# Performance work log

Measured on AMD Instinct MI355X. Metric: run time of the kernel, lower is better.

The kernel has to match this reference:

```python
import jax, jax.numpy as jnp
import numpy as np
from jax import lax

N_NODES = 100000
N_EDGES = 600000  # even: edges stored as consecutive reverse pairs
NODE_F = 64
EDGE_F = 16
EDGE_H = 128
NODE_H = 128
NUM_STEPS = 6


def setup_inputs() -> dict:
    key = jax.random.key(0)
    ks = jax.random.split(key, 16)
    # paired reverse edges: edge 2k is (src,dst), edge 2k+1 is (dst,src)
    src = jax.random.randint(ks[0], (N_EDGES // 2,), 0, N_NODES, dtype=jnp.int32)
    dst = jax.random.randint(ks[1], (N_EDGES // 2,), 0, N_NODES, dtype=jnp.int32)
    from_nodes = jnp.stack([src, dst], axis=1).reshape(-1)
    to_nodes = jnp.stack([dst, src], axis=1).reshape(-1)
    edges = jnp.stack([from_nodes, to_nodes], axis=0)
    return {
        "node_features": jax.random.normal(ks[2], (N_NODES, NODE_F), jnp.float32),
        "edge_features": jax.random.normal(ks[3], (N_EDGES, EDGE_F), jnp.float32),
        "edge_hiddens": jnp.zeros((N_EDGES, EDGE_H), jnp.float32),
        "edges": edges,
        "W1_w": jax.random.normal(ks[4], (NODE_F, EDGE_H), jnp.float32) / np.sqrt(NODE_F),
        "W1_b": jnp.zeros((EDGE_H,), jnp.float32),
        "W2_w": jax.random.normal(ks[5], (EDGE_F, EDGE_H), jnp.float32) / np.sqrt(EDGE_F),
        "W2_b": jnp.zeros((EDGE_H,), jnp.float32),
        "W3_w": jax.random.normal(ks[6], (EDGE_H, EDGE_H), jnp.float32) / np.sqrt(EDGE_H),
        "W3_b": jnp.zeros((EDGE_H,), jnp.float32),
        "U1_w": jax.random.normal(ks[7], (NODE_F, NODE_H), jnp.float32) / np.sqrt(NODE_F),
        "U1_b": jnp.zeros((NODE_H,), jnp.float32),
        "U2_w": jax.random.normal(ks[8], (EDGE_H, NODE_H), jnp.float32) / np.sqrt(EDGE_H),
        "U2_b": jnp.zeros((NODE_H,), jnp.float32),
    }


def reference(node_features, edge_features, edge_hiddens, edges,
              W1_w, W1_b, W2_w, W2_b, W3_w, W3_b, U1_w, U1_b, U2_w, U2_b):
    from_nodes = edges[0]
    to_nodes = edges[1]
    n_edges = edges.shape[1]
    # backlink of edge i is its reverse pair: even i -> i+1, odd i -> i-1
    idx = jnp.arange(n_edges)
    backlink = idx + ((idx + 1) % 2) * 2 - 1

    # loop-invariant terms
    W1_x_u = (node_features @ W1_w + W1_b)[from_nodes]     # [E, EH]
    W2_x_uv = edge_features @ W2_w + W2_b                  # [E, EH]

    def step(h, _):
        # sum edge hiddens by source node, gather back per-edge, drop backlink
        s = jax.ops.segment_sum(h, from_nodes, num_segments=N_NODES)  # [N, EH]
        wu = s[from_nodes] - h[backlink]                               # [E, EH]
        h_new = jax.nn.relu(W1_x_u + W2_x_uv + (wu @ W3_w + W3_b))
        return h_new, None

    edge_h, _ = lax.scan(step, edge_hiddens, None, length=NUM_STEPS)

    U1_x_u = node_features @ U1_w + U1_b                   # [N, NH]
    U2_vu = edge_h @ U2_w + U2_b                           # [E, NH]
    agg = jax.ops.segment_sum(U2_vu, to_nodes, num_segments=N_NODES)
    node_hiddens = jax.nn.relu(U1_x_u + agg)               # [N, NH]
    return node_hiddens
```

## Files before the change

kernel.cpp:

```cpp
#include <hip/hip_runtime.h>
#include <hip/hip_bf16.h>

#define N_NODES 100000
#define N_EDGES 600000
#define SCAN_BLOCKS ((N_NODES + 255) / 256)

typedef __bf16 bf16;
typedef __bf16 bf16x2 __attribute__((ext_vector_type(2)));
typedef __bf16 bf16x4 __attribute__((ext_vector_type(4)));
typedef __bf16 bf16x8 __attribute__((ext_vector_type(8)));
typedef float f32x4 __attribute__((ext_vector_type(4)));

__global__ void deg_hist(const int* __restrict__ from, int* __restrict__ deg, int E) {
    int e = blockIdx.x * blockDim.x + threadIdx.x;
    if (e < E) atomicAdd(&deg[from[e]], 1);
}

__global__ __launch_bounds__(256) void block_sums(
    const int* __restrict__ deg, int* __restrict__ bsum)
{
    __shared__ int s[256];
    int i = blockIdx.x * 256 + threadIdx.x;
    s[threadIdx.x] = (i < N_NODES) ? deg[i] : 0;
    __syncthreads();
    for (int st = 128; st > 0; st >>= 1) {
        if (threadIdx.x < st) s[threadIdx.x] += s[threadIdx.x + st];
        __syncthreads();
    }
    if (threadIdx.x == 0) bsum[blockIdx.x] = s[0];
}

__global__ __launch_bounds__(256) void scan_partials(
    const int* __restrict__ bsum, int* __restrict__ bpref, int* __restrict__ off)
{
    __shared__ int s[SCAN_BLOCKS];
    for (int i = threadIdx.x; i < SCAN_BLOCKS; i += 256) s[i] = bsum[i];
    __syncthreads();
    if (threadIdx.x == 0) {
        int run = 0;
        for (int i = 0; i < SCAN_BLOCKS; i++) { int t = s[i]; s[i] = run; run += t; }
        off[N_NODES] = run;
    }
    __syncthreads();
    for (int i = threadIdx.x; i < SCAN_BLOCKS; i += 256) bpref[i] = s[i];
}

__global__ __launch_bounds__(256) void block_scan(
    const int* __restrict__ deg, const int* __restrict__ bpref,
    int* __restrict__ off, int* __restrict__ cursor)
{
    __shared__ int s[256];
    int i = blockIdx.x * 256 + threadIdx.x;
    int v = (i < N_NODES) ? deg[i] : 0;
    s[threadIdx.x] = v;
    __syncthreads();
    for (int st = 1; st < 256; st <<= 1) {
        int x = (threadIdx.x >= st) ? s[threadIdx.x - st] : 0;
        __syncthreads();
        s[threadIdx.x] += x;
        __syncthreads();
    }
    if (i < N_NODES) {
        int o = bpref[blockIdx.x] + s[threadIdx.x] - v;
        off[i] = o;
        cursor[i] = o;
    }
}

__global__ void scatter_csr(const int* __restrict__ from, int* __restrict__ cursor,
                            int* __restrict__ se, int* __restrict__ rank, int E) {
    int e = blockIdx.x * blockDim.x + threadIdx.x;
    if (e < E) {
        int p = atomicAdd(&cursor[from[e]], 1);
        se[p] = e;
        rank[e] = p;
    }
}

__global__ void make_maps(const int* __restrict__ se, const int* __restrict__ from,
                          const int* __restrict__ rank,
                          int* __restrict__ fromP, int* __restrict__ backP, int E) {
    int i = blockIdx.x * blockDim.x + threadIdx.x;
    if (i < E) {
        int e = se[i];
        fromP[i] = from[e];
        backP[i] = rank[e ^ 1];
    }
}

__global__ __launch_bounds__(256) void node_gemm(
    const float* __restrict__ A, const float* __restrict__ B,
    const float* __restrict__ bias, float* __restrict__ C, int M)
{
    __shared__ float As[16][65];
    __shared__ float Bs[16][128];
    int row0 = blockIdx.x * 64;
    int tid = threadIdx.x;
    int tx = tid & 15, ty = tid >> 4;
    float acc[4][8];
    #pragma unroll
    for (int i = 0; i < 4; i++)
        #pragma unroll
        for (int j = 0; j < 8; j++) acc[i][j] = 0.f;

    for (int kk = 0; kk < 64; kk += 16) {
        int m  = tid >> 2;
        int k4 = (tid & 3) * 4;
        float4 v = make_float4(0.f, 0.f, 0.f, 0.f);
        if (row0 + m < M)
            v = *(const float4*)(A + (size_t)(row0 + m) * 64 + kk + k4);
        As[k4 + 0][m] = v.x; As[k4 + 1][m] = v.y;
        As[k4 + 2][m] = v.z; As[k4 + 3][m] = v.w;
        #pragma unroll
        for (int t = 0; t < 2; t++) {
            int id = tid + t * 256;
            int k = id >> 5, n4 = (id & 31) * 4;
            *(float4*)(&Bs[k][n4]) = *(const float4*)(B + (size_t)(kk + k) * 128 + n4);
        }
        __syncthreads();
        #pragma unroll
        for (int k = 0; k < 16; k++) {
            float a[4], b[8];
            #pragma unroll
            for (int i = 0; i < 4; i++) a[i] = As[k][ty * 4 + i];
            #pragma unroll
            for (int j = 0; j < 8; j++) b[j] = Bs[k][tx + j * 16];
            #pragma unroll
            for (int i = 0; i < 4; i++)
                #pragma unroll
                for (int j = 0; j < 8; j++) acc[i][j] += a[i] * b[j];
        }
        __syncthreads();
    }
    #pragma unroll
    for (int i = 0; i < 4; i++) {
        int r = row0 + ty * 4 + i;
        if (r < M) {
            #pragma unroll
            for (int j = 0; j < 8; j++) {
                int c = tx + j * 16;
                C[(size_t)r * 128 + c] = acc[i][j] + bias[c];
            }
        }
    }
}

__global__ __launch_bounds__(256) void base_sorted(
    const float* __restrict__ nodeW1, const int* __restrict__ fromP,
    const int* __restrict__ se, const float* __restrict__ ef,
    const float* __restrict__ W2, const float* __restrict__ W2b,
    const float* __restrict__ W3b, bf16* __restrict__ baseP)
{
    int tid = threadIdx.x;
    int c0 = (tid & 31) * 4;
    int sub = tid >> 5;
    float4 w[16];
    #pragma unroll
    for (int k = 0; k < 16; k++) w[k] = *(const float4*)(W2 + k * 128 + c0);
    float4 bias;
    {
        float4 a = *(const float4*)(W2b + c0);
        float4 b = *(const float4*)(W3b + c0);
        bias = make_float4(a.x + b.x, a.y + b.y, a.z + b.z, a.w + b.w);
    }
    #pragma unroll 1
    for (int it = 0; it < 64; ++it) {
        int i = blockIdx.x * 512 + it * 8 + sub;
        if (i >= N_EDGES) break;
        const float* efr = ef + (size_t)se[i] * 16;
        float4 nv = *(const float4*)(nodeW1 + (size_t)fromP[i] * 128 + c0);
        float4 acc = make_float4(bias.x + nv.x, bias.y + nv.y,
                                 bias.z + nv.z, bias.w + nv.w);
        #pragma unroll
        for (int k = 0; k < 16; k++) {
            float s = efr[k];
            acc.x += s * w[k].x; acc.y += s * w[k].y;
            acc.z += s * w[k].z; acc.w += s * w[k].w;
        }
        bf16x4 o;
        o[0] = (bf16)acc.x; o[1] = (bf16)acc.y; o[2] = (bf16)acc.z; o[3] = (bf16)acc.w;
        *(bf16x4*)(baseP + (size_t)i * 128 + c0) = o;
    }
}

__global__ __launch_bounds__(256) void prep_weights(
    const float* __restrict__ W3, const float* __restrict__ U2,
    bf16* __restrict__ W3T, bf16* __restrict__ U2T)
{
    int i = blockIdx.x * 256 + threadIdx.x;
    if (i < 128 * 128) {
        int k = i >> 7, n = i & 127;
        W3T[n * 128 + k] = (bf16)W3[k * 128 + n];
        U2T[n * 128 + k] = (bf16)U2[k * 128 + n];
    }
}

__global__ __launch_bounds__(256) void edge_mfma_v2(
    const bf16* __restrict__ baseP, const bf16* __restrict__ gin,
    const bf16* __restrict__ S, const int* __restrict__ fromP,
    const int* __restrict__ backP, const bf16* __restrict__ BT,
    bf16* __restrict__ gout, int fused)
{
    __shared__ bf16 Bsw[128 * 128];
    int tid = threadIdx.x;

    #pragma unroll
    for (int t = 0; t < 8; t++) {
        int c = tid + t * 256;
        int cmr = c & 15;
        int cq  = (c >> 4) & 3;
        int ckt = (c >> 6) & 3;
        int cn  = c >> 8;
        int brow = cn * 16 + cmr;
        int bcol = ckt * 32 + cq * 8;
        *(bf16x8*)&Bsw[(size_t)c * 8] =
            *(const bf16x8*)(BT + (size_t)brow * 128 + bcol);
    }
    __syncthreads();

    int wave = tid >> 6, lane = tid & 63;
    int quad = lane >> 4, mr = lane & 15;

    #pragma unroll 1
    for (int it = 0; it < 4; ++it) {
        int i0 = blockIdx.x * 256 + wave * 64 + it * 16;
        if (i0 >= N_EDGES) break;
        int i = i0 + mr;

        bf16x8 afr[4];
        if (!fused) {
            #pragma unroll
            for (int kt = 0; kt < 4; kt++) {
                bf16x8 bb = *(const bf16x8*)(baseP + (size_t)i * 128 + kt * 32 + quad * 8);
                #pragma unroll
                for (int j = 0; j < 8; j++)
                    afr[kt][j] = (bf16)fmaxf((float)bb[j], 0.f);
            }
        } else {
            const bf16* sr = S   + (size_t)fromP[i] * 128;
            const bf16* gr = gin + (size_t)backP[i] * 128;
            #pragma unroll
            for (int kt = 0; kt < 4; kt++) {
                int c = kt * 32 + quad * 8;
                bf16x8 bb = *(const bf16x8*)(baseP + (size_t)i * 128 + c);
                bf16x8 gg = *(const bf16x8*)(gr + c);
                bf16x8 ss = *(const bf16x8*)(sr + c);
                #pragma unroll
                for (int j = 0; j < 8; j++) {
                    float v = (float)bb[j] + (float)ss[j] - (float)gg[j];
                    afr[kt][j] = (bf16)fmaxf(v, 0.f);
                }
            }
        }

        f32x4 acc[8];
        #pragma unroll
        for (int n = 0; n < 8; n++) acc[n] = (f32x4){0.f, 0.f, 0.f, 0.f};
        #pragma unroll
        for (int kt = 0; kt < 4; kt++) {
            #pragma unroll
            for (int n = 0; n < 8; n++) {
                bf16x8 b = *(const bf16x8*)&Bsw[(size_t)(((n * 4 + kt) * 64) + lane) * 8];
                acc[n] = __builtin_amdgcn_mfma_f32_16x16x32_bf16(afr[kt], b, acc[n], 0, 0, 0);
            }
        }

        #pragma unroll
        for (int np = 0; np < 4; np++) {
            int n0 = np * 2;
            #pragma unroll
            for (int reg = 0; reg < 4; reg++) {
                float v0 = acc[n0][reg], v1 = acc[n0 + 1][reg];
                float o0 = __shfl_xor(v0, 1);
                float o1 = __shfl_xor(v1, 1);
                bf16x2 pk;
                int colb;
                if ((mr & 1) == 0) {
                    pk[0] = (bf16)v0; pk[1] = (bf16)o0;
                    colb = n0 * 16 + mr;
                } else {
                    pk[0] = (bf16)o1; pk[1] = (bf16)v1;
                    colb = (n0 + 1) * 16 + (mr ^ 1);
                }
                int row = i0 + quad * 4 + reg;
                *(bf16x2*)(gout + (size_t)row * 128 + colb) = pk;
            }
        }
    }
}

__global__ __launch_bounds__(256) void segsum_stream(
    const bf16* __restrict__ g, const int* __restrict__ off, bf16* __restrict__ S)
{
    int n = blockIdx.x * 4 + (threadIdx.x >> 6);
    if (n >= N_NODES) return;
    int lane = threadIdx.x & 63;
    int o0 = off[n], o1 = off[n + 1];
    float a0 = 0.f, a1 = 0.f;
    for (int i = o0; i < o1; ++i) {
        bf16x2 v = *(const bf16x2*)(g + (size_t)i * 128 + lane * 2);
        a0 += (float)v[0];
        a1 += (float)v[1];
    }
    bf16x2 o; o[0] = (bf16)a0; o[1] = (bf16)a1;
    *(bf16x2*)(S + (size_t)n * 128 + lane * 2) = o;
}

__global__ __launch_bounds__(256) void segsum_final(
    const bf16* __restrict__ g, const int* __restrict__ off,
    const int* __restrict__ backP, float* __restrict__ agg)
{
    int n = blockIdx.x * 4 + (threadIdx.x >> 6);
    if (n >= N_NODES) return;
    int lane = threadIdx.x & 63;
    int o0 = off[n], o1 = off[n + 1];
    float a0 = 0.f, a1 = 0.f;
    for (int i = o0; i < o1; ++i) {
        int e = backP[i];
        bf16x2 v = *(const bf16x2*)(g + (size_t)e * 128 + lane * 2);
        a0 += (float)v[0];
        a1 += (float)v[1];
    }
    *(float2*)(agg + (size_t)n * 128 + lane * 2) = make_float2(a0, a1);
}

__global__ __launch_bounds__(256) void final_out(
    const float* __restrict__ U1x, const float* __restrict__ agg,
    const int* __restrict__ deg, const float* __restrict__ U2b,
    float* __restrict__ out)
{
    int gid = blockIdx.x * 256 + threadIdx.x;
    int n  = gid >> 5;
    if (n >= N_NODES) return;
    int c4 = gid & 31;
    float d = (float)deg[n];
    float4 a  = *(const float4*)(U1x + (size_t)n * 128 + c4 * 4);
    float4 ag = *(const float4*)(agg + (size_t)n * 128 + c4 * 4);
    float4 ub = *(const float4*)(U2b + c4 * 4);
    float4 r;
    r.x = fmaxf(a.x + ag.x + d * ub.x, 0.f);
    r.y = fmaxf(a.y + ag.y + d * ub.y, 0.f);
    r.z = fmaxf(a.z + ag.z + d * ub.z, 0.f);
    r.w = fmaxf(a.w + ag.w + d * ub.w, 0.f);
    *(float4*)(out + (size_t)n * 128 + c4 * 4) = r;
}

extern "C" void kernel_launch(void* const* d_in, const int* in_sizes, int n_in,
                              void* d_out, int out_size, void* d_ws, size_t ws_size,
                              hipStream_t stream) {
    const float* nf  = (const float*)d_in[0];
    const float* ef  = (const float*)d_in[1];
    const int* edges = (const int*)d_in[3];
    const int* from  = edges;
    const float* W1w = (const float*)d_in[4];
    const float* W1b = (const float*)d_in[5];
    const float* W2w = (const float*)d_in[6];
    const float* W2b = (const float*)d_in[7];
    const float* W3w = (const float*)d_in[8];
    const float* W3b = (const float*)d_in[9];
    const float* U1w = (const float*)d_in[10];
    const float* U1b = (const float*)d_in[11];
    const float* U2w = (const float*)d_in[12];
    const float* U2b = (const float*)d_in[13];
    float* out = (float*)d_out;

    const size_t NODE_MAT = (size_t)N_NODES * 128;
    const size_t EDGE_MAT = (size_t)N_EDGES * 128;
    char* w = (char*)d_ws;
    float* nodeW1 = (float*)w; w += NODE_MAT * 4;
    float* agg    = (float*)w; w += NODE_MAT * 4;
    bf16*  S      = (bf16*)w;  w += NODE_MAT * 2;
    bf16*  baseP  = (bf16*)w;  w += EDGE_MAT * 2;
    bf16*  g0     = (bf16*)w;  w += EDGE_MAT * 2;
    bf16*  g1     = (bf16*)w;  w += EDGE_MAT * 2;
    bf16*  W3T    = (bf16*)w;  w += 128 * 128 * 2;
    bf16*  U2T    = (bf16*)w;  w += 128 * 128 * 2;
    int*   deg    = (int*)w;   w += (size_t)N_NODES * 4;
    int*   off    = (int*)w;   w += (size_t)(N_NODES + 1) * 4;
    int*   cursor = (int*)w;   w += (size_t)N_NODES * 4;
    int*   bsum   = (int*)w;   w += (size_t)SCAN_BLOCKS * 4;
    int*   bpref  = (int*)w;   w += (size_t)SCAN_BLOCKS * 4;
    int*   se     = (int*)w;   w += (size_t)N_EDGES * 4;
    int*   rank   = (int*)w;   w += (size_t)N_EDGES * 4;
    int*   fromP  = (int*)w;   w += (size_t)N_EDGES * 4;
    int*   backP  = (int*)w;   w += (size_t)N_EDGES * 4;

    hipMemsetAsync(deg, 0, (size_t)N_NODES * 4, stream);
    deg_hist<<<(N_EDGES + 255) / 256, 256, 0, stream>>>(from, deg, N_EDGES);
    block_sums<<<SCAN_BLOCKS, 256, 0, stream>>>(deg, bsum);
    scan_partials<<<1, 256, 0, stream>>>(bsum, bpref, off);
    block_scan<<<SCAN_BLOCKS, 256, 0, stream>>>(deg, bpref, off, cursor);
    scatter_csr<<<(N_EDGES + 255) / 256, 256, 0, stream>>>(from, cursor, se, rank, N_EDGES);
    make_maps<<<(N_EDGES + 255) / 256, 256, 0, stream>>>(se, from, rank, fromP, backP, N_EDGES);

    prep_weights<<<(128 * 128 + 255) / 256, 256, 0, stream>>>(W3w, U2w, W3T, U2T);
    node_gemm<<<(N_NODES + 63) / 64, 256, 0, stream>>>(nf, W1w, W1b, nodeW1, N_NODES);
    base_sorted<<<(N_EDGES + 511) / 512, 256, 0, stream>>>(
        nodeW1, fromP, se, ef, W2w, W2b, W3b, baseP);

    const int EGRID = (N_EDGES + 255) / 256;
    bf16* G[2] = {g0, g1};
    edge_mfma_v2<<<EGRID, 256, 0, stream>>>(
        baseP, G[0], S, fromP, backP, W3T, G[0], 0);
    segsum_stream<<<(N_NODES + 3) / 4, 256, 0, stream>>>(G[0], off, S);
    int cur = 0;
    for (int it = 1; it < 5; ++it) {
        edge_mfma_v2<<<EGRID, 256, 0, stream>>>(
            baseP, G[cur], S, fromP, backP, W3T, G[cur ^ 1], 1);
        cur ^= 1;
        segsum_stream<<<(N_NODES + 3) / 4, 256, 0, stream>>>(G[cur], off, S);
    }
    edge_mfma_v2<<<EGRID, 256, 0, stream>>>(
        baseP, G[cur], S, fromP, backP, U2T, G[cur ^ 1], 1);
    cur ^= 1;
    segsum_final<<<(N_NODES + 3) / 4, 256, 0, stream>>>(G[cur], off, backP, agg);

    node_gemm<<<(N_NODES + 63) / 64, 256, 0, stream>>>(nf, U1w, U1b, nodeW1, N_NODES);
    final_out<<<(N_NODES * 32 + 255) / 256, 256, 0, stream>>>(nodeW1, agg, deg, U2b, out);
}
```

Baseline: 1.657 ms.

## Fuse segment sums into edge MFMA kernel with fp32 atomic boundary accumulation

Each per-step segment-sum kernel is folded into the edge GEMM kernel's epilogue. After a block writes its sorted edge rows, each wave re-reads its 64 rows and reduces contiguous runs per source node into an fp32 node buffer, using plain stores for runs fully inside the wave and atomics at boundaries. Double-buffered fp32 node sums are zeroed with memsets between steps. The last GEMM scatters rows through backP so the final aggregation reads contiguously, and the final reduction is fused with the U1 add, degree bias and ReLU. This removes separate kernel launches and some passes over edge data, but adds memsets, fp32 gathers that are twice as large, and atomics.

```diff
diff --git a/kernel.cpp b/kernel.cpp
--- a/kernel.cpp
+++ b/kernel.cpp
@@ -195,11 +195,12 @@
     }
 }
 
-__global__ __launch_bounds__(256) void edge_mfma_v2(
+__global__ __launch_bounds__(256) void edge_mfma_v3(
     const bf16* __restrict__ baseP, const bf16* __restrict__ gin,
-    const bf16* __restrict__ S, const int* __restrict__ fromP,
-    const int* __restrict__ backP, const bf16* __restrict__ BT,
-    bf16* __restrict__ gout, int fused)
+    const float* __restrict__ Sin, const int* __restrict__ fromP,
+    const int* __restrict__ backP, const int* __restrict__ off,
+    const bf16* __restrict__ BT, bf16* __restrict__ gout,
+    float* __restrict__ Sout, int fused, int do_seg, int scatter)
 {
     __shared__ bf16 Bsw[128 * 128];
     int tid = threadIdx.x;
@@ -237,17 +238,19 @@
                     afr[kt][j] = (bf16)fmaxf((float)bb[j], 0.f);
             }
         } else {
-            const bf16* sr = S   + (size_t)fromP[i] * 128;
-            const bf16* gr = gin + (size_t)backP[i] * 128;
+            const float* sr = Sin + (size_t)fromP[i] * 128;
+            const bf16*  gr = gin + (size_t)backP[i] * 128;
             #pragma unroll
             for (int kt = 0; kt < 4; kt++) {
                 int c = kt * 32 + quad * 8;
                 bf16x8 bb = *(const bf16x8*)(baseP + (size_t)i * 128 + c);
                 bf16x8 gg = *(const bf16x8*)(gr + c);
-                bf16x8 ss = *(const bf16x8*)(sr + c);
+                float4 s0 = *(const float4*)(sr + c);
+                float4 s1 = *(const float4*)(sr + c + 4);
+                float sv[8] = {s0.x, s0.y, s0.z, s0.w, s1.x, s1.y, s1.z, s1.w};
                 #pragma unroll
                 for (int j = 0; j < 8; j++) {
-                    float v = (float)bb[j] + (float)ss[j] - (float)gg[j];
+                    float v = (float)bb[j] + sv[j] - (float)gg[j];
                     afr[kt][j] = (bf16)fmaxf(v, 0.f);
                 }
             }
@@ -264,6 +267,12 @@
                 acc[n] = __builtin_amdgcn_mfma_f32_16x16x32_bf16(afr[kt], b, acc[n], 0, 0, 0);
             }
         }
+
+        int rbase4 = i0 + quad * 4;
+        int orow[4];
+        #pragma unroll
+        for (int reg = 0; reg < 4; reg++)
+            orow[reg] = scatter ? backP[rbase4 + reg] : (rbase4 + reg);
 
         #pragma unroll
         for (int np = 0; np < 4; np++) {
@@ -282,15 +291,43 @@
                     pk[0] = (bf16)o1; pk[1] = (bf16)v1;
                     colb = (n0 + 1) * 16 + (mr ^ 1);
                 }
-                int row = i0 + quad * 4 + reg;
-                *(bf16x2*)(gout + (size_t)row * 128 + colb) = pk;
-            }
-        }
-    }
-}
-
-__global__ __launch_bounds__(256) void segsum_stream(
-    const bf16* __restrict__ g, const int* __restrict__ off, bf16* __restrict__ S)
+                *(bf16x2*)(gout + (size_t)orow[reg] * 128 + colb) = pk;
+            }
+        }
+    }
+
+    if (do_seg) {
+        __syncthreads();
+        int rbase = blockIdx.x * 256 + wave * 64;
+        int rend  = rbase + 64;
+        if (rend > N_EDGES) rend = N_EDGES;
+        int r = rbase;
+        while (r < rend) {
+            int n  = fromP[r];
+            int bs = off[n], be = off[n + 1];
+            int e  = be < rend ? be : rend;
+            float a0 = 0.f, a1 = 0.f;
+            for (int j = r; j < e; ++j) {
+                bf16x2 v = *(const bf16x2*)(gout + (size_t)j * 128 + lane * 2);
+                a0 += (float)v[0];
+                a1 += (float)v[1];
+            }
+            float* sp = Sout + (size_t)n * 128 + lane * 2;
+            if (bs >= rbase && be <= rend) {
+                *(float2*)sp = make_float2(a0, a1);
+            } else {
+                atomicAdd(sp, a0);
+                atomicAdd(sp + 1, a1);
+            }
+            r = e;
+        }
+    }
+}
+
+__global__ __launch_bounds__(256) void segsum_final_fused(
+    const bf16* __restrict__ gB, const int* __restrict__ off,
+    const float* __restrict__ U1x, const float* __restrict__ U2b,
+    float* __restrict__ out)
 {
     int n = blockIdx.x * 4 + (threadIdx.x >> 6);
     if (n >= N_NODES) return;
@@ -298,51 +335,16 @@
     int o0 = off[n], o1 = off[n + 1];
     float a0 = 0.f, a1 = 0.f;
     for (int i = o0; i < o1; ++i) {
-        bf16x2 v = *(const bf16x2*)(g + (size_t)i * 128 + lane * 2);
+        bf16x2 v = *(const bf16x2*)(gB + (size_t)i * 128 + lane * 2);
         a0 += (float)v[0];
         a1 += (float)v[1];
     }
-    bf16x2 o; o[0] = (bf16)a0; o[1] = (bf16)a1;
-    *(bf16x2*)(S + (size_t)n * 128 + lane * 2) = o;
-}
-
-__global__ __launch_bounds__(256) void segsum_final(
-    const bf16* __restrict__ g, const int* __restrict__ off,
-    const int* __restrict__ backP, float* __restrict__ agg)
-{
-    int n = blockIdx.x * 4 + (threadIdx.x >> 6);
-    if (n >= N_NODES) return;
-    int lane = threadIdx.x & 63;
-    int o0 = off[n], o1 = off[n + 1];
-    float a0 = 0.f, a1 = 0.f;
-    for (int i = o0; i < o1; ++i) {
-        int e = backP[i];
-        bf16x2 v = *(const bf16x2*)(g + (size_t)e * 128 + lane * 2);
-        a0 += (float)v[0];
-        a1 += (float)v[1];
-    }
-    *(float2*)(agg + (size_t)n * 128 + lane * 2) = make_float2(a0, a1);
-}
-
-__global__ __launch_bounds__(256) void final_out(
-    const float* __restrict__ U1x, const float* __restrict__ agg,
-    const int* __restrict__ deg, const float* __restrict__ U2b,
-    float* __restrict__ out)
-{
-    int gid = blockIdx.x * 256 + threadIdx.x;
-    int n  = gid >> 5;
-    if (n >= N_NODES) return;
-    int c4 = gid & 31;
-    float d = (float)deg[n];
-    float4 a  = *(const float4*)(U1x + (size_t)n * 128 + c4 * 4);
-    float4 ag = *(const float4*)(agg + (size_t)n * 128 + c4 * 4);
-    float4 ub = *(const float4*)(U2b + c4 * 4);
-    float4 r;
-    r.x = fmaxf(a.x + ag.x + d * ub.x, 0.f);
-    r.y = fmaxf(a.y + ag.y + d * ub.y, 0.f);
-    r.z = fmaxf(a.z + ag.z + d * ub.z, 0.f);
-    r.w = fmaxf(a.w + ag.w + d * ub.w, 0.f);
-    *(float4*)(out + (size_t)n * 128 + c4 * 4) = r;
+    float d = (float)(o1 - o0);
+    float2 u = *(const float2*)(U1x + (size_t)n * 128 + lane * 2);
+    float2 b = *(const float2*)(U2b + lane * 2);
+    float r0 = fmaxf(u.x + a0 + d * b.x, 0.f);
+    float r1 = fmaxf(u.y + a1 + d * b.y, 0.f);
+    *(float2*)(out + (size_t)n * 128 + lane * 2) = make_float2(r0, r1);
 }
 
 extern "C" void kernel_launch(void* const* d_in, const int* in_sizes, int n_in,
@@ -368,8 +370,8 @@
     const size_t EDGE_MAT = (size_t)N_EDGES * 128;
     char* w = (char*)d_ws;
     float* nodeW1 = (float*)w; w += NODE_MAT * 4;
-    float* agg    = (float*)w; w += NODE_MAT * 4;
-    bf16*  S      = (bf16*)w;  w += NODE_MAT * 2;
+    float* SA     = (float*)w; w += NODE_MAT * 4;
+    float* SB     = (float*)w; w += NODE_MAT * 4;
     bf16*  baseP  = (bf16*)w;  w += EDGE_MAT * 2;
     bf16*  g0     = (bf16*)w;  w += EDGE_MAT * 2;
     bf16*  g1     = (bf16*)w;  w += EDGE_MAT * 2;
@@ -399,22 +401,28 @@
         nodeW1, fromP, se, ef, W2w, W2b, W3b, baseP);
 
     const int EGRID = (N_EDGES + 255) / 256;
-    bf16* G[2] = {g0, g1};
-    edge_mfma_v2<<<EGRID, 256, 0, stream>>>(
-        baseP, G[0], S, fromP, backP, W3T, G[0], 0);
-    segsum_stream<<<(N_NODES + 3) / 4, 256, 0, stream>>>(G[0], off, S);
-    int cur = 0;
-    for (int it = 1; it < 5; ++it) {
-        edge_mfma_v2<<<EGRID, 256, 0, stream>>>(
-            baseP, G[cur], S, fromP, backP, W3T, G[cur ^ 1], 1);
-        cur ^= 1;
-        segsum_stream<<<(N_NODES + 3) / 4, 256, 0, stream>>>(G[cur], off, S);
-    }
-    edge_mfma_v2<<<EGRID, 256, 0, stream>>>(
-        baseP, G[cur], S, fromP, backP, U2T, G[cur ^ 1], 1);
-    cur ^= 1;
-    segsum_final<<<(N_NODES + 3) / 4, 256, 0, stream>>>(G[cur], off, backP, agg);
+    const size_t SBYTES = NODE_MAT * 4;
+
+    hipMemsetAsync(SA, 0, SBYTES, stream);
+    edge_mfma_v3<<<EGRID, 256, 0, stream>>>(
+        baseP, g0, SB, fromP, backP, off, W3T, g0, SA, 0, 1, 0);
+    hipMemsetAsync(SB, 0, SBYTES, stream);
+    edge_mfma_v3<<<EGRID, 256, 0, stream>>>(
+        baseP, g0, SA, fromP, backP, off, W3T, g1, SB, 1, 1, 0);
+    hipMemsetAsync(SA, 0, SBYTES, stream);
+    edge_mfma_v3<<<EGRID, 256, 0, stream>>>(
+        baseP, g1, SB, fromP, backP, off, W3T, g0, SA, 1, 1, 0);
+    hipMemsetAsync(SB, 0, SBYTES, stream);
+    edge_mfma_v3<<<EGRID, 256, 0, stream>>>(
+        baseP, g0, SA, fromP, backP, off, W3T, g1, SB, 1, 1, 0);
+    hipMemsetAsync(SA, 0, SBYTES, stream);
+    edge_mfma_v3<<<EGRID, 256, 0, stream>>>(
+        baseP, g1, SB, fromP, backP, off, W3T, g0, SA, 1, 1, 0);
+
+    edge_mfma_v3<<<EGRID, 256, 0, stream>>>(
+        baseP, g0, SA, fromP, backP, off, U2T, g1, SB, 1, 0, 1);
 
     node_gemm<<<(N_NODES + 63) / 64, 256, 0, stream>>>(nf, U1w, U1b, nodeW1, N_NODES);
-    final_out<<<(N_NODES * 32 + 255) / 256, 256, 0, stream>>>(nodeW1, agg, deg, U2b, out);
-}
+    segsum_final_fused<<<(N_NODES + 3) / 4, 256, 0, stream>>>(
+        g1, off, nodeW1, U2b, out);
+}
```

Result: slower. 1.936 ms (+16.8%).

## Keep edges in original order and gather by sorted index in segment sums

Applied to the files above, without the earlier changes.

Edge hidden buffers now stay in the original edge order instead of CSR-sorted order. The backlink becomes i^1, so the make_maps kernel and the rank/fromP/backP arrays go away. The segment sums now gather rows through the sorted edge list instead of streaming contiguous rows. The final segment sum is also fused with the output epilogue, which removes the agg buffer and one kernel. In exchange, the per-node segsum reads become scattered rather than contiguous, while the edge kernel's backlink read becomes adjacent.

```diff
diff --git a/kernel.cpp b/kernel.cpp
--- a/kernel.cpp
+++ b/kernel.cpp
@@ -68,23 +68,11 @@
 }
 
 __global__ void scatter_csr(const int* __restrict__ from, int* __restrict__ cursor,
-                            int* __restrict__ se, int* __restrict__ rank, int E) {
+                            int* __restrict__ se, int E) {
     int e = blockIdx.x * blockDim.x + threadIdx.x;
     if (e < E) {
         int p = atomicAdd(&cursor[from[e]], 1);
         se[p] = e;
-        rank[e] = p;
-    }
-}
-
-__global__ void make_maps(const int* __restrict__ se, const int* __restrict__ from,
-                          const int* __restrict__ rank,
-                          int* __restrict__ fromP, int* __restrict__ backP, int E) {
-    int i = blockIdx.x * blockDim.x + threadIdx.x;
-    if (i < E) {
-        int e = se[i];
-        fromP[i] = from[e];
-        backP[i] = rank[e ^ 1];
     }
 }
 
@@ -145,11 +133,11 @@
     }
 }
 
-__global__ __launch_bounds__(256) void base_sorted(
-    const float* __restrict__ nodeW1, const int* __restrict__ fromP,
-    const int* __restrict__ se, const float* __restrict__ ef,
-    const float* __restrict__ W2, const float* __restrict__ W2b,
-    const float* __restrict__ W3b, bf16* __restrict__ baseP)
+__global__ __launch_bounds__(256) void base_orig(
+    const float* __restrict__ nodeW1, const int* __restrict__ from,
+    const float* __restrict__ ef, const float* __restrict__ W2,
+    const float* __restrict__ W2b, const float* __restrict__ W3b,
+    bf16* __restrict__ base)
 {
     int tid = threadIdx.x;
     int c0 = (tid & 31) * 4;
@@ -167,8 +155,8 @@
     for (int it = 0; it < 64; ++it) {
         int i = blockIdx.x * 512 + it * 8 + sub;
         if (i >= N_EDGES) break;
-        const float* efr = ef + (size_t)se[i] * 16;
-        float4 nv = *(const float4*)(nodeW1 + (size_t)fromP[i] * 128 + c0);
+        const float* efr = ef + (size_t)i * 16;
+        float4 nv = *(const float4*)(nodeW1 + (size_t)from[i] * 128 + c0);
         float4 acc = make_float4(bias.x + nv.x, bias.y + nv.y,
                                  bias.z + nv.z, bias.w + nv.w);
         #pragma unroll
@@ -179,7 +167,7 @@
         }
         bf16x4 o;
         o[0] = (bf16)acc.x; o[1] = (bf16)acc.y; o[2] = (bf16)acc.z; o[3] = (bf16)acc.w;
-        *(bf16x4*)(baseP + (size_t)i * 128 + c0) = o;
+        *(bf16x4*)(base + (size_t)i * 128 + c0) = o;
     }
 }
 
@@ -195,11 +183,10 @@
     }
 }
 
-__global__ __launch_bounds__(256) void edge_mfma_v2(
-    const bf16* __restrict__ baseP, const bf16* __restrict__ gin,
-    const bf16* __restrict__ S, const int* __restrict__ fromP,
-    const int* __restrict__ backP, const bf16* __restrict__ BT,
-    bf16* __restrict__ gout, int fused)
+__global__ __launch_bounds__(256) void edge_mfma_v4(
+    const bf16* __restrict__ base, const bf16* __restrict__ gin,
+    const bf16* __restrict__ S, const int* __restrict__ from,
+    const bf16* __restrict__ BT, bf16* __restrict__ gout, int fused)
 {
     __shared__ bf16 Bsw[128 * 128];
     int tid = threadIdx.x;
@@ -231,18 +218,18 @@
         if (!fused) {
             #pragma unroll
             for (int kt = 0; kt < 4; kt++) {
-                bf16x8 bb = *(const bf16x8*)(baseP + (size_t)i * 128 + kt * 32 + quad * 8);
+                bf16x8 bb = *(const bf16x8*)(base + (size_t)i * 128 + kt * 32 + quad * 8);
                 #pragma unroll
                 for (int j = 0; j < 8; j++)
                     afr[kt][j] = (bf16)fmaxf((float)bb[j], 0.f);
             }
         } else {
-            const bf16* sr = S   + (size_t)fromP[i] * 128;
-            const bf16* gr = gin + (size_t)backP[i] * 128;
+            const bf16* sr = S   + (size_t)from[i] * 128;
+            const bf16* gr = gin + (size_t)(i ^ 1) * 128;
             #pragma unroll
             for (int kt = 0; kt < 4; kt++) {
                 int c = kt * 32 + quad * 8;
-                bf16x8 bb = *(const bf16x8*)(baseP + (size_t)i * 128 + c);
+                bf16x8 bb = *(const bf16x8*)(base + (size_t)i * 128 + c);
                 bf16x8 gg = *(const bf16x8*)(gr + c);
                 bf16x8 ss = *(const bf16x8*)(sr + c);
                 #pragma unroll
@@ -289,16 +276,18 @@
     }
 }
 
-__global__ __launch_bounds__(256) void segsum_stream(
-    const bf16* __restrict__ g, const int* __restrict__ off, bf16* __restrict__ S)
+__global__ __launch_bounds__(256) void segsum_gather(
+    const bf16* __restrict__ g, const int* __restrict__ se,
+    const int* __restrict__ off, bf16* __restrict__ S)
 {
     int n = blockIdx.x * 4 + (threadIdx.x >> 6);
     if (n >= N_NODES) return;
     int lane = threadIdx.x & 63;
     int o0 = off[n], o1 = off[n + 1];
     float a0 = 0.f, a1 = 0.f;
-    for (int i = o0; i < o1; ++i) {
-        bf16x2 v = *(const bf16x2*)(g + (size_t)i * 128 + lane * 2);
+    for (int p = o0; p < o1; ++p) {
+        int e = se[p];
+        bf16x2 v = *(const bf16x2*)(g + (size_t)e * 128 + lane * 2);
         a0 += (float)v[0];
         a1 += (float)v[1];
     }
@@ -306,43 +295,28 @@
     *(bf16x2*)(S + (size_t)n * 128 + lane * 2) = o;
 }
 
-__global__ __launch_bounds__(256) void segsum_final(
-    const bf16* __restrict__ g, const int* __restrict__ off,
-    const int* __restrict__ backP, float* __restrict__ agg)
+__global__ __launch_bounds__(256) void final_gather_out(
+    const bf16* __restrict__ gB, const int* __restrict__ se,
+    const int* __restrict__ off, const float* __restrict__ U1x,
+    const float* __restrict__ U2b, float* __restrict__ out)
 {
     int n = blockIdx.x * 4 + (threadIdx.x >> 6);
     if (n >= N_NODES) return;
     int lane = threadIdx.x & 63;
     int o0 = off[n], o1 = off[n + 1];
     float a0 = 0.f, a1 = 0.f;
-    for (int i = o0; i < o1; ++i) {
-        int e = backP[i];
-        bf16x2 v = *(const bf16x2*)(g + (size_t)e * 128 + lane * 2);
+    for (int p = o0; p < o1; ++p) {
+        int e = se[p] ^ 1;
+        bf16x2 v = *(const bf16x2*)(gB + (size_t)e * 128 + lane * 2);
         a0 += (float)v[0];
         a1 += (float)v[1];
     }
-    *(float2*)(agg + (size_t)n * 128 + lane * 2) = make_float2(a0, a1);
-}
-
-__global__ __launch_bounds__(256) void final_out(
-    const float* __restrict__ U1x, const float* __restrict__ agg,
-    const int* __restrict__ deg, const float* __restrict__ U2b,
-    float* __restrict__ out)
-{
-    int gid = blockIdx.x * 256 + threadIdx.x;
-    int n  = gid >> 5;
-    if (n >= N_NODES) return;
-    int c4 = gid & 31;
-    float d = (float)deg[n];
-    float4 a  = *(const float4*)(U1x + (size_t)n * 128 + c4 * 4);
-    float4 ag = *(const float4*)(agg + (size_t)n * 128 + c4 * 4);
-    float4 ub = *(const float4*)(U2b + c4 * 4);
-    float4 r;
-    r.x = fmaxf(a.x + ag.x + d * ub.x, 0.f);
-    r.y = fmaxf(a.y + ag.y + d * ub.y, 0.f);
-    r.z = fmaxf(a.z + ag.z + d * ub.z, 0.f);
-    r.w = fmaxf(a.w + ag.w + d * ub.w, 0.f);
-    *(float4*)(out + (size_t)n * 128 + c4 * 4) = r;
+    float d = (float)(o1 - o0);
+    float2 u = *(const float2*)(U1x + (size_t)n * 128 + lane * 2);
+    float2 b = *(const float2*)(U2b + lane * 2);
+    float r0 = fmaxf(u.x + a0 + d * b.x, 0.f);
+    float r1 = fmaxf(u.y + a1 + d * b.y, 0.f);
+    *(float2*)(out + (size_t)n * 128 + lane * 2) = make_float2(r0, r1);
 }
 
 extern "C" void kernel_launch(void* const* d_in, const int* in_sizes, int n_in,
@@ -368,9 +342,8 @@
     const size_t EDGE_MAT = (size_t)N_EDGES * 128;
     char* w = (char*)d_ws;
     float* nodeW1 = (float*)w; w += NODE_MAT * 4;
-    float* agg    = (float*)w; w += NODE_MAT * 4;
     bf16*  S      = (bf16*)w;  w += NODE_MAT * 2;
-    bf16*  baseP  = (bf16*)w;  w += EDGE_MAT * 2;
+    bf16*  base   = (bf16*)w;  w += EDGE_MAT * 2;
     bf16*  g0     = (bf16*)w;  w += EDGE_MAT * 2;
     bf16*  g1     = (bf16*)w;  w += EDGE_MAT * 2;
     bf16*  W3T    = (bf16*)w;  w += 128 * 128 * 2;
@@ -381,40 +354,34 @@
     int*   bsum   = (int*)w;   w += (size_t)SCAN_BLOCKS * 4;
     int*   bpref  = (int*)w;   w += (size_t)SCAN_BLOCKS * 4;
     int*   se     = (int*)w;   w += (size_t)N_EDGES * 4;
-    int*   rank   = (int*)w;   w += (size_t)N_EDGES * 4;
-    int*   fromP  = (int*)w;   w += (size_t)N_EDGES * 4;
-    int*   backP  = (int*)w;   w += (size_t)N_EDGES * 4;
 
     hipMemsetAsync(deg, 0, (size_t)N_NODES * 4, stream);
     deg_hist<<<(N_EDGES + 255) / 256, 256, 0, stream>>>(from, deg, N_EDGES);
     block_sums<<<SCAN_BLOCKS, 256, 0, stream>>>(deg, bsum);
     scan_partials<<<1, 256, 0, stream>>>(bsum, bpref, off);
     block_scan<<<SCAN_BLOCKS, 256, 0, stream>>>(deg, bpref, off, cursor);
-    scatter_csr<<<(N_EDGES + 255) / 256, 256, 0, stream>>>(from, cursor, se, rank, N_EDGES);
-    make_maps<<<(N_EDGES + 255) / 256, 256, 0, stream>>>(se, from, rank, fromP, backP, N_EDGES);
+    scatter_csr<<<(N_EDGES + 255) / 256, 256, 0, stream>>>(from, cursor, se, N_EDGES);
 
     prep_weights<<<(128 * 128 + 255) / 256, 256, 0, stream>>>(W3w, U2w, W3T, U2T);
     node_gemm<<<(N_NODES + 63) / 64, 256, 0, stream>>>(nf, W1w, W1b, nodeW1, N_NODES);
-    base_sorted<<<(N_EDGES + 511) / 512, 256, 0, stream>>>(
-        nodeW1, fromP, se, ef, W2w, W2b, W3b, baseP);
+    base_orig<<<(N_EDGES + 511) / 512, 256, 0, stream>>>(
+        nodeW1, from, ef, W2w, W2b, W3b, base);
 
     const int EGRID = (N_EDGES + 255) / 256;
+    const int SGRID = (N_NODES + 3) / 4;
     bf16* G[2] = {g0, g1};
-    edge_mfma_v2<<<EGRID, 256, 0, stream>>>(
-        baseP, G[0], S, fromP, backP, W3T, G[0], 0);
-    segsum_stream<<<(N_NODES + 3) / 4, 256, 0, stream>>>(G[0], off, S);
+
+    edge_mfma_v4<<<EGRID, 256, 0, stream>>>(base, G[0], S, from, W3T, G[0], 0);
+    segsum_gather<<<SGRID, 256, 0, stream>>>(G[0], se, off, S);
     int cur = 0;
     for (int it = 1; it < 5; ++it) {
-        edge_mfma_v2<<<EGRID, 256, 0, stream>>>(
-            baseP, G[cur], S, fromP, backP, W3T, G[cur ^ 1], 1);
+        edge_mfma_v4<<<EGRID, 256, 0, stream>>>(base, G[cur], S, from, W3T, G[cur ^ 1], 1);
         cur ^= 1;
-        segsum_stream<<<(N_NODES + 3) / 4, 256, 0, stream>>>(G[cur], off, S);
-    }
-    edge_mfma_v2<<<EGRID, 256, 0, stream>>>(
-        baseP, G[cur], S, fromP, backP, U2T, G[cur ^ 1], 1);
+        segsum_gather<<<SGRID, 256, 0, stream>>>(G[cur], se, off, S);
+    }
+    edge_mfma_v4<<<EGRID, 256, 0, stream>>>(base, G[cur], S, from, U2T, G[cur ^ 1], 1);
     cur ^= 1;
-    segsum_final<<<(N_NODES + 3) / 4, 256, 0, stream>>>(G[cur], off, backP, agg);
 
     node_gemm<<<(N_NODES + 63) / 64, 256, 0, stream>>>(nf, U1w, U1b, nodeW1, N_NODES);
-    final_out<<<(N_NODES * 32 + 255) / 256, 256, 0, stream>>>(nodeW1, agg, deg, U2b, out);
-}
+    final_gather_out<<<SGRID, 256, 0, stream>>>(G[cur], se, off, nodeW1, U2b, out);
+}
```

New measurement: 1.852 ms. 11.8% more time.

## Scatter backlink rows during segsum so edge GEMM reads them contiguously

Applied to the files above, without the earlier changes.

The segment-sum kernel now also writes each edge hidden row to its backlink position in a second buffer. The edge MFMA kernel can then read the back-edge term sequentially instead of through an indirect gather. The last edge GEMM scatters its output rows by backlink, so the final aggregation streams contiguous rows and fuses the U1/bias/ReLU epilogue, which removes the agg buffer and a separate kernel. The cost is an extra scattered write pass of an edge matrix in every segsum.

```diff
diff --git a/kernel.cpp b/kernel.cpp
--- a/kernel.cpp
+++ b/kernel.cpp
@@ -195,11 +195,11 @@
     }
 }
 
-__global__ __launch_bounds__(256) void edge_mfma_v2(
-    const bf16* __restrict__ baseP, const bf16* __restrict__ gin,
+__global__ __launch_bounds__(256) void edge_mfma_v5(
+    const bf16* __restrict__ baseP, const bf16* __restrict__ gBP,
     const bf16* __restrict__ S, const int* __restrict__ fromP,
     const int* __restrict__ backP, const bf16* __restrict__ BT,
-    bf16* __restrict__ gout, int fused)
+    bf16* __restrict__ gout, int fused, int scatter)
 {
     __shared__ bf16 Bsw[128 * 128];
     int tid = threadIdx.x;
@@ -238,7 +238,7 @@
             }
         } else {
             const bf16* sr = S   + (size_t)fromP[i] * 128;
-            const bf16* gr = gin + (size_t)backP[i] * 128;
+            const bf16* gr = gBP + (size_t)i * 128;
             #pragma unroll
             for (int kt = 0; kt < 4; kt++) {
                 int c = kt * 32 + quad * 8;
@@ -264,6 +264,12 @@
                 acc[n] = __builtin_amdgcn_mfma_f32_16x16x32_bf16(afr[kt], b, acc[n], 0, 0, 0);
             }
         }
+
+        int rbase4 = i0 + quad * 4;
+        int orow[4];
+        #pragma unroll
+        for (int reg = 0; reg < 4; reg++)
+            orow[reg] = scatter ? backP[rbase4 + reg] : (rbase4 + reg);
 
         #pragma unroll
         for (int np = 0; np < 4; np++) {
@@ -282,67 +288,54 @@
                     pk[0] = (bf16)o1; pk[1] = (bf16)v1;
                     colb = (n0 + 1) * 16 + (mr ^ 1);
                 }
-                int row = i0 + quad * 4 + reg;
-                *(bf16x2*)(gout + (size_t)row * 128 + colb) = pk;
+                *(bf16x2*)(gout + (size_t)orow[reg] * 128 + colb) = pk;
             }
         }
     }
 }
 
-__global__ __launch_bounds__(256) void segsum_stream(
-    const bf16* __restrict__ g, const int* __restrict__ off, bf16* __restrict__ S)
+__global__ __launch_bounds__(256) void segsum_scatter(
+    const bf16* __restrict__ g, const int* __restrict__ backP,
+    const int* __restrict__ off, bf16* __restrict__ S,
+    bf16* __restrict__ gBPout)
 {
     int n = blockIdx.x * 4 + (threadIdx.x >> 6);
     if (n >= N_NODES) return;
     int lane = threadIdx.x & 63;
     int o0 = off[n], o1 = off[n + 1];
     float a0 = 0.f, a1 = 0.f;
-    for (int i = o0; i < o1; ++i) {
-        bf16x2 v = *(const bf16x2*)(g + (size_t)i * 128 + lane * 2);
+    for (int p = o0; p < o1; ++p) {
+        bf16x2 v = *(const bf16x2*)(g + (size_t)p * 128 + lane * 2);
         a0 += (float)v[0];
         a1 += (float)v[1];
+        int q = backP[p];
+        *(bf16x2*)(gBPout + (size_t)q * 128 + lane * 2) = v;
     }
     bf16x2 o; o[0] = (bf16)a0; o[1] = (bf16)a1;
     *(bf16x2*)(S + (size_t)n * 128 + lane * 2) = o;
 }
 
-__global__ __launch_bounds__(256) void segsum_final(
-    const bf16* __restrict__ g, const int* __restrict__ off,
-    const int* __restrict__ backP, float* __restrict__ agg)
+__global__ __launch_bounds__(256) void final_out_stream(
+    const bf16* __restrict__ X, const int* __restrict__ off,
+    const float* __restrict__ U1x, const float* __restrict__ U2b,
+    float* __restrict__ out)
 {
     int n = blockIdx.x * 4 + (threadIdx.x >> 6);
     if (n >= N_NODES) return;
     int lane = threadIdx.x & 63;
     int o0 = off[n], o1 = off[n + 1];
     float a0 = 0.f, a1 = 0.f;
-    for (int i = o0; i < o1; ++i) {
-        int e = backP[i];
-        bf16x2 v = *(const bf16x2*)(g + (size_t)e * 128 + lane * 2);
+    for (int p = o0; p < o1; ++p) {
+        bf16x2 v = *(const bf16x2*)(X + (size_t)p * 128 + lane * 2);
         a0 += (float)v[0];
         a1 += (float)v[1];
     }
-    *(float2*)(agg + (size_t)n * 128 + lane * 2) = make_float2(a0, a1);
-}
-
-__global__ __launch_bounds__(256) void final_out(
-    const float* __restrict__ U1x, const float* __restrict__ agg,
-    const int* __restrict__ deg, const float* __restrict__ U2b,
-    float* __restrict__ out)
-{
-    int gid = blockIdx.x * 256 + threadIdx.x;
-    int n  = gid >> 5;
-    if (n >= N_NODES) return;
-    int c4 = gid & 31;
-    float d = (float)deg[n];
-    float4 a  = *(const float4*)(U1x + (size_t)n * 128 + c4 * 4);
-    float4 ag = *(const float4*)(agg + (size_t)n * 128 + c4 * 4);
-    float4 ub = *(const float4*)(U2b + c4 * 4);
-    float4 r;
-    r.x = fmaxf(a.x + ag.x + d * ub.x, 0.f);
-    r.y = fmaxf(a.y + ag.y + d * ub.y, 0.f);
-    r.z = fmaxf(a.z + ag.z + d * ub.z, 0.f);
-    r.w = fmaxf(a.w + ag.w + d * ub.w, 0.f);
-    *(float4*)(out + (size_t)n * 128 + c4 * 4) = r;
+    float d = (float)(o1 - o0);
+    float2 u = *(const float2*)(U1x + (size_t)n * 128 + lane * 2);
+    float2 b = *(const float2*)(U2b + lane * 2);
+    float r0 = fmaxf(u.x + a0 + d * b.x, 0.f);
+    float r1 = fmaxf(u.y + a1 + d * b.y, 0.f);
+    *(float2*)(out + (size_t)n * 128 + lane * 2) = make_float2(r0, r1);
 }
 
 extern "C" void kernel_launch(void* const* d_in, const int* in_sizes, int n_in,
@@ -368,11 +361,10 @@
     const size_t EDGE_MAT = (size_t)N_EDGES * 128;
     char* w = (char*)d_ws;
     float* nodeW1 = (float*)w; w += NODE_MAT * 4;
-    float* agg    = (float*)w; w += NODE_MAT * 4;
     bf16*  S      = (bf16*)w;  w += NODE_MAT * 2;
     bf16*  baseP  = (bf16*)w;  w += EDGE_MAT * 2;
-    bf16*  g0     = (bf16*)w;  w += EDGE_MAT * 2;
-    bf16*  g1     = (bf16*)w;  w += EDGE_MAT * 2;
+    bf16*  G      = (bf16*)w;  w += EDGE_MAT * 2;
+    bf16*  GBP    = (bf16*)w;  w += EDGE_MAT * 2;
     bf16*  W3T    = (bf16*)w;  w += 128 * 128 * 2;
     bf16*  U2T    = (bf16*)w;  w += 128 * 128 * 2;
     int*   deg    = (int*)w;   w += (size_t)N_NODES * 4;
@@ -399,22 +391,19 @@
         nodeW1, fromP, se, ef, W2w, W2b, W3b, baseP);
 
     const int EGRID = (N_EDGES + 255) / 256;
-    bf16* G[2] = {g0, g1};
-    edge_mfma_v2<<<EGRID, 256, 0, stream>>>(
-        baseP, G[0], S, fromP, backP, W3T, G[0], 0);
-    segsum_stream<<<(N_NODES + 3) / 4, 256, 0, stream>>>(G[0], off, S);
-    int cur = 0;
+    const int SGRID = (N_NODES + 3) / 4;
+
+    edge_mfma_v5<<<EGRID, 256, 0, stream>>>(
+        baseP, GBP, S, fromP, backP, W3T, G, 0, 0);
+    segsum_scatter<<<SGRID, 256, 0, stream>>>(G, backP, off, S, GBP);
     for (int it = 1; it < 5; ++it) {
-        edge_mfma_v2<<<EGRID, 256, 0, stream>>>(
-            baseP, G[cur], S, fromP, backP, W3T, G[cur ^ 1], 1);
-        cur ^= 1;
-        segsum_stream<<<(N_NODES + 3) / 4, 256, 0, stream>>>(G[cur], off, S);
-    }
-    edge_mfma_v2<<<EGRID, 256, 0, stream>>>(
-        baseP, G[cur], S, fromP, backP, U2T, G[cur ^ 1], 1);
-    cur ^= 1;
-    segsum_final<<<(N_NODES + 3) / 4, 256, 0, stream>>>(G[cur], off, backP, agg);
+        edge_mfma_v5<<<EGRID, 256, 0, stream>>>(
+            baseP, GBP, S, fromP, backP, W3T, G, 1, 0);
+        segsum_scatter<<<SGRID, 256, 0, stream>>>(G, backP, off, S, GBP);
+    }
+    edge_mfma_v5<<<EGRID, 256, 0, stream>>>(
+        baseP, GBP, S, fromP, backP, U2T, G, 1, 1);
 
     node_gemm<<<(N_NODES + 63) / 64, 256, 0, stream>>>(nf, U1w, U1b, nodeW1, N_NODES);
-    final_out<<<(N_NODES * 32 + 255) / 256, 256, 0, stream>>>(nodeW1, agg, deg, U2b, out);
-}
+    final_out_stream<<<SGRID, 256, 0, stream>>>(G, off, nodeW1, U2b, out);
+}
```

New measurement: 1.815 ms. +9.6%, slower.
